# Kernel optimization log

Hardware: AMD Instinct MI355X
Metric: run time of the kernel (lower is better)

Reference implementation:

```python
import jax, jax.numpy as jnp
import numpy as np

DIM = 192
HEADS = 6
HEAD_DIM = DIM // HEADS
WS = 8            # window size
N = WS * WS       # tokens per window
IN_CC = 16        # top-k kept keys per query
B, H, W = 8, 64, 64
NEG = -100.0      # value used by the torch code for masked logits
EPS_NORM = 1e-12  # F.normalize eps
EPS_LN = 1e-5     # nn.LayerNorm eps


def _rel_pos_index(ws):
    coords = np.stack(np.meshgrid(np.arange(ws), np.arange(ws), indexing='ij'))  # (2,ws,ws)
    cf = coords.reshape(2, -1)
    rel = (cf[:, :, None] - cf[:, None, :]).transpose(1, 2, 0).astype(np.int64)  # (N,N,2)
    rel[:, :, 0] += ws - 1
    rel[:, :, 1] += ws - 1
    rel[:, :, 0] *= 2 * ws - 1
    return jnp.asarray(rel.sum(-1))  # (N,N) indices into (2ws-1)^2 table

REL_IDX = _rel_pos_index(WS)


def _layer_norm(x, g, b):
    mu = jnp.mean(x, -1, keepdims=True)
    var = jnp.mean(jnp.square(x - mu), -1, keepdims=True)
    return (x - mu) * jax.lax.rsqrt(var + EPS_LN) * g + b


def _l2n(x):
    n = jnp.sqrt(jnp.sum(jnp.square(x), -1, keepdims=True))
    return x / jnp.maximum(n, EPS_NORM)


def setup_inputs() -> dict:
    key = jax.random.key(0)
    ks = jax.random.split(key, 8)
    s = 0.02
    return {
        'x': jax.random.normal(ks[0], (B, DIM, H, W), jnp.float32),
        'norm1_g': jnp.ones((DIM,), jnp.float32),
        'norm1_b': jnp.zeros((DIM,), jnp.float32),
        'qkv_w': jax.random.normal(ks[1], (3 * DIM, DIM), jnp.float32) * s,
        'qkv_b': jnp.zeros((3 * DIM,), jnp.float32),
        'proj_w': jax.random.normal(ks[2], (DIM, DIM), jnp.float32) * s,
        'proj_b': jnp.zeros((DIM,), jnp.float32),
        'rpb_table': jax.random.normal(ks[3], ((2 * WS - 1) ** 2, HEADS), jnp.float32) * s,
        'temperature': jnp.ones((HEADS, 1, 1), jnp.float32),
        'norm2_g': jnp.ones((DIM,), jnp.float32),
        'norm2_b': jnp.zeros((DIM,), jnp.float32),
        'fc1_w': jax.random.normal(ks[4], (4 * DIM, DIM), jnp.float32) * s,
        'fc1_b': jnp.zeros((4 * DIM,), jnp.float32),
        'fc2_w': jax.random.normal(ks[5], (DIM, 4 * DIM), jnp.float32) * s,
        'fc2_b': jnp.zeros((DIM,), jnp.float32),
    }


def reference(x, norm1_g, norm1_b, qkv_w, qkv_b, proj_w, proj_b, rpb_table,
              temperature, norm2_g, norm2_b, fc1_w, fc1_b, fc2_w, fc2_b):
    b, c, h, w = x.shape
    # (B,C,H,W) -> (B,L,C), pre-norm (note: the torch code norms the shortcut too)
    xs = jnp.transpose(x.reshape(b, c, h * w), (0, 2, 1))
    shortcut = _layer_norm(xs, norm1_g, norm1_b)  # (B,L,C)

    # window partition: (B,H,W,C) -> (B*nWh*nWw, N, C); shift_size=0, no padding (H,W % WS == 0)
    xin = shortcut.reshape(b, h // WS, WS, w // WS, WS, c)
    xin = jnp.transpose(xin, (0, 1, 3, 2, 4, 5)).reshape(-1, N, c)
    B_ = xin.shape[0]

    qkv = (xin @ qkv_w.T + qkv_b).reshape(B_, N, 3, HEADS, HEAD_DIM)
    qkv = jnp.transpose(qkv, (2, 0, 3, 1, 4))  # (3, B_, h, N, d)
    q, k, v = qkv[0], qkv[1], qkv[2]

    # cosine attention with learned per-head temperature
    attn = jnp.einsum('bhnd,bhmd->bhnm', _l2n(q), _l2n(k)) * temperature  # (B_,h,N,N)

    # top-k sparsification: keep IN_CC largest logits per query (threshold == kth value;
    # equivalent to the torch topk+scatter mask for distinct values)
    kth = jax.lax.top_k(attn, IN_CC)[0][..., -1:]
    attn = jnp.where(attn >= kth, attn, NEG)

    # relative position bias gather: (N,N,h) -> (h,N,N)
    rpb = jnp.transpose(rpb_table[REL_IDX], (2, 0, 1))
    attn = jax.nn.softmax(attn + rpb[None], axis=-1)

    out = jnp.einsum('bhnm,bhmd->bhnd', attn, v)
    out = jnp.transpose(out, (0, 2, 1, 3)).reshape(B_, N, c)
    out = out @ proj_w.T + proj_b

    # window reverse -> (B, L, C)
    out = out.reshape(b, h // WS, w // WS, WS, WS, c)
    out = jnp.transpose(out, (0, 1, 3, 2, 4, 5)).reshape(b, h * w, c)

    x2 = shortcut + out  # drop_path = identity (eval)
    hdn = _layer_norm(x2, norm2_g, norm2_b)
    hdn = jax.nn.gelu(hdn @ fc1_w.T + fc1_b, approximate=False) @ fc2_w.T + fc2_b
    x2 = x2 + hdn

    # back to (B,C,H,W)
    return jnp.transpose(x2, (0, 2, 1)).reshape(b, c, h, w)
```

## Files before the change

### kernel.cpp

```cpp
#include <hip/hip_runtime.h>
#include <hip/hip_bf16.h>
#include <math.h>

#define DIM     192
#define HEADS   6
#define HEAD_DIM 32
#define NTOK    64
#define IN_CC   16
#define TTOT    32768
#define NWIN    512

using bf16x8 = __attribute__((ext_vector_type(8))) short;
using f32x4  = __attribute__((ext_vector_type(4))) float;
typedef unsigned short ushort_t;

__device__ __forceinline__ ushort_t f2b(float f) {
    unsigned u = __float_as_uint(f);
    u += 0x7fffu + ((u >> 16) & 1u);
    return (ushort_t)(u >> 16);
}
__device__ __forceinline__ unsigned pk2(float a, float b) {
    return (unsigned)f2b(a) | ((unsigned)f2b(b) << 16);
}
__device__ __forceinline__ float b2f(ushort_t u) {
    return __uint_as_float(((unsigned)u) << 16);
}

__global__ __launch_bounds__(256) void cvt_all_kernel(
    const float* __restrict__ s0, const float* __restrict__ s1,
    const float* __restrict__ s2, const float* __restrict__ s3,
    ushort_t* __restrict__ d0, ushort_t* __restrict__ d1,
    ushort_t* __restrict__ d2, ushort_t* __restrict__ d3)
{
    const int bid = blockIdx.x;
    const float* src; ushort_t* dst; int off, K;
    if (bid < 108)      { src = s0; dst = d0; off = bid;       K = 192; }
    else if (bid < 144) { src = s1; dst = d1; off = bid - 108; K = 192; }
    else if (bid < 288) { src = s2; dst = d2; off = bid - 144; K = 192; }
    else                { src = s3; dst = d3; off = bid - 288; K = 768; }
    const int K8 = K >> 3;
    const int d  = (off * 256 + threadIdx.x) * 4;
    const int frag = d >> 7, win = d & 127;
    const int m16w = win >> 3, k7 = win & 7;
    const int oblk = frag / K8, kblk = frag - oblk * K8;
    const int o = oblk * 16 + m16w, k = kblk * 8 + k7;
    float4 v = *(const float4*)(src + (size_t)o * K + k);
    ushort4 ov;
    ov.x = f2b(v.x); ov.y = f2b(v.y); ov.z = f2b(v.z); ov.w = f2b(v.w);
    *(ushort4*)(dst + d) = ov;
}

__global__ __launch_bounds__(256) void ln1_kernel(
    const float* __restrict__ x, const float* __restrict__ g,
    const float* __restrict__ bb, ushort_t* __restrict__ outh)
{
    __shared__ float xs[64][193];
    __shared__ float mu_s[64], rs_s[64];
    __shared__ float gs[192], bs[192];
    const int tid = threadIdx.x;
    const int t0  = blockIdx.x * 64;
    const int b   = t0 >> 12;
    const int hw0 = t0 & 4095;
    if (tid < 192) { gs[tid] = g[tid]; bs[tid] = bb[tid]; }
    const int tok = tid & 63, qq = tid >> 6;
    const float* xb = x + (size_t)b * (DIM * 4096) + hw0 + tok;
    #pragma unroll
    for (int it = 0; it < 48; ++it) {
        int c = it * 4 + qq;
        xs[tok][c] = xb[(size_t)c * 4096];
    }
    __syncthreads();
    const int tok2 = tid >> 2, p = tid & 3;
    float sum = 0.f;
    #pragma unroll
    for (int c = 0; c < 48; ++c) sum += xs[tok2][p * 48 + c];
    sum += __shfl_xor(sum, 1);
    sum += __shfl_xor(sum, 2);
    const float m = sum * (1.0f / 192.0f);
    float ss = 0.f;
    #pragma unroll
    for (int c = 0; c < 48; ++c) { float d = xs[tok2][p * 48 + c] - m; ss += d * d; }
    ss += __shfl_xor(ss, 1);
    ss += __shfl_xor(ss, 2);
    if (p == 0) {
        mu_s[tok2] = m;
        rs_s[tok2] = 1.0f / sqrtf(ss * (1.0f / 192.0f) + 1e-5f);
    }
    __syncthreads();
    ushort_t* obh = outh + (size_t)t0 * DIM;
    #pragma unroll
    for (int it = 0; it < 48; ++it) {
        int idx = it * 256 + tid;
        int tk = idx / 192, c = idx % 192;
        obh[idx] = f2b((xs[tk][c] - mu_s[tk]) * rs_s[tk] * gs[c] + bs[c]);
    }
}

__global__ __launch_bounds__(384) void attn_fused(
    const ushort_t* __restrict__ sc_h, const ushort_t* __restrict__ wqf,
    const float* __restrict__ qkv_b, const float* __restrict__ rpb_table,
    const float* __restrict__ temp, const ushort_t* __restrict__ wpf,
    const float* __restrict__ proj_b, float* __restrict__ x2)
{
    __shared__ __align__(16) char smem[98304];
    const int tid  = threadIdx.x;
    const int wave = tid >> 6, n = tid & 63;
    char* arena = smem + wave * 16384;
    ushort_t* Qh  = (ushort_t*)arena;
    ushort_t* Kh  = (ushort_t*)(arena + 5120);
    float*    Ss  = (float*)arena;
    ushort_t* Pl  = (ushort_t*)arena;
    ushort_t* Vt  = (ushort_t*)(arena + 10240);
    float*    ksb = (float*)(arena + 14848);
    float*    qnb = (float*)(arena + 15104);
    float*    rpb = (float*)(arena + 15360);
    ushort_t (*AoT)[200] = (ushort_t(*)[200])smem;
    float* Cww = (float*)(smem + 25600 + wave * 9216);

    const int win = blockIdx.x;
    const int h   = wave;
    const int b   = win >> 6;
    const int wh  = (win >> 3) & 7, ww = win & 7;
    const int i1  = n >> 3, j1 = n & 7;
    const int m16 = n & 15, quad = n >> 4;

    for (int r = n; r < 225; r += 64) rpb[r] = rpb_table[r * 6 + h];

    int trow[4];
    #pragma unroll
    for (int i = 0; i < 4; ++i) {
        const int row = 16 * i + m16;
        trow[i] = b * 4096 + (wh * 8 + (row >> 3)) * 64 + ww * 8 + (row & 7);
    }

    #pragma unroll
    for (int part = 0; part < 3; ++part) {
        const int o0 = part * 192 + h * 32;
        f32x4 pa[4][2];
        #pragma unroll
        for (int i = 0; i < 4; ++i)
            #pragma unroll
            for (int j = 0; j < 2; ++j)
                pa[i][j] = (f32x4)(0.0f);
        const ushort_t* Wb = wqf + (size_t)(o0 >> 4) * 24 * 128 + m16 * 8;
        for (int ks = 0; ks < 192; ks += 32) {
            bf16x8 af[4], wv[2];
            #pragma unroll
            for (int i = 0; i < 4; ++i)
                af[i] = *(const bf16x8*)(sc_h + (size_t)trow[i] * 192 + ks + quad * 8);
            #pragma unroll
            for (int j = 0; j < 2; ++j)
                wv[j] = *(const bf16x8*)(Wb + (size_t)(j * 24 + (ks >> 3) + quad) * 128);
            #pragma unroll
            for (int i = 0; i < 4; ++i)
                #pragma unroll
                for (int j = 0; j < 2; ++j)
                    pa[i][j] = __builtin_amdgcn_mfma_f32_16x16x32_bf16(wv[j], af[i], pa[i][j], 0, 0, 0);
        }
        float4 bv0 = *(const float4*)&qkv_b[o0 + quad * 4];
        float4 bv1 = *(const float4*)&qkv_b[o0 + 16 + quad * 4];
        float ssq[4] = {0.f, 0.f, 0.f, 0.f};
        #pragma unroll
        for (int i = 0; i < 4; ++i) {
            f32x4 v0 = pa[i][0], v1 = pa[i][1];
            v0[0] += bv0.x; v0[1] += bv0.y; v0[2] += bv0.z; v0[3] += bv0.w;
            v1[0] += bv1.x; v1[1] += bv1.y; v1[2] += bv1.z; v1[3] += bv1.w;
            if (part < 2) {
                #pragma unroll
                for (int r = 0; r < 4; ++r)
                    ssq[i] += v0[r] * v0[r] + v1[r] * v1[r];
                ushort_t* dst = (part == 0) ? Qh : Kh;
                uint2 w0, w1;
                w0.x = pk2(v0[0], v0[1]); w0.y = pk2(v0[2], v0[3]);
                w1.x = pk2(v1[0], v1[1]); w1.y = pk2(v1[2], v1[3]);
                *(uint2*)&dst[(16 * i + m16) * 40 + quad * 4]      = w0;
                *(uint2*)&dst[(16 * i + m16) * 40 + 16 + quad * 4] = w1;
            } else {
                #pragma unroll
                for (int r = 0; r < 4; ++r) {
                    Vt[(quad * 4 + r) * 72 + 4 * m16 + i]      = f2b(v0[r]);
                    Vt[(16 + quad * 4 + r) * 72 + 4 * m16 + i] = f2b(v1[r]);
                }
            }
        }
        if (part < 2) {
            #pragma unroll
            for (int i = 0; i < 4; ++i) {
                ssq[i] += __shfl_xor(ssq[i], 16);
                ssq[i] += __shfl_xor(ssq[i], 32);
            }
            if (quad == 0) {
                #pragma unroll
                for (int i = 0; i < 4; ++i) {
                    if (part == 0) qnb[16 * i + m16] = ssq[i];
                    else           ksb[4 * m16 + i]  = 1.0f / fmaxf(sqrtf(ssq[i]), 1e-12f);
                }
            }
        }
    }

    bf16x8 aq[4], bk[4];
    #pragma unroll
    for (int i = 0; i < 4; ++i) aq[i] = *(const bf16x8*)&Qh[(16*i + m16) * 40 + quad * 8];
    #pragma unroll
    for (int j = 0; j < 4; ++j) bk[j] = *(const bf16x8*)&Kh[(16*j + m16) * 40 + quad * 8];
    f32x4 acc[4][4];
    #pragma unroll
    for (int i = 0; i < 4; ++i)
        #pragma unroll
        for (int j = 0; j < 4; ++j)
            acc[i][j] = __builtin_amdgcn_mfma_f32_16x16x32_bf16(aq[i], bk[j], (f32x4)(0.0f), 0, 0, 0);

    float s[64];
    #pragma unroll
    for (int i = 0; i < 2; ++i)
        #pragma unroll
        for (int r = 0; r < 4; ++r) {
            f32x4 vv = { acc[i][0][r], acc[i][1][r], acc[i][2][r], acc[i][3][r] };
            *(f32x4*)&Ss[(16 * i + 4 * quad + r) * 68 + 4 * m16] = vv;
        }
    if (n < 32) {
        #pragma unroll
        for (int c = 0; c < 16; ++c)
            *(float4*)&s[4 * c] = *(const float4*)&Ss[n * 68 + 4 * c];
    }
    #pragma unroll
    for (int i = 2; i < 4; ++i)
        #pragma unroll
        for (int r = 0; r < 4; ++r) {
            f32x4 vv = { acc[i][0][r], acc[i][1][r], acc[i][2][r], acc[i][3][r] };
            *(f32x4*)&Ss[(16 * (i - 2) + 4 * quad + r) * 68 + 4 * m16] = vv;
        }
    if (n >= 32) {
        #pragma unroll
        for (int c = 0; c < 16; ++c)
            *(float4*)&s[4 * c] = *(const float4*)&Ss[(n - 32) * 68 + 4 * c];
    }

    const float qs = temp[h] / fmaxf(sqrtf(qnb[n]), 1e-12f);
    #pragma unroll
    for (int c = 0; c < 16; ++c) {
        float4 kv = *(const float4*)&ksb[4 * c];
        s[4*c+0] *= qs * kv.x; s[4*c+1] *= qs * kv.y;
        s[4*c+2] *= qs * kv.z; s[4*c+3] *= qs * kv.w;
    }

    float thr = 1e30f;
    for (int it = 0; it < IN_CC; ++it) {
        float mx = -1e30f;
        #pragma unroll
        for (int m = 0; m < 64; ++m) {
            float vv = (s[m] < thr) ? s[m] : -1e30f;
            mx = fmaxf(mx, vv);
        }
        thr = mx;
    }

    const int basen = i1 * 15 + j1;
    float mx = -1e30f;
    #pragma unroll
    for (int c = 0; c < 64; ++c) {
        const int m = 16 * (c & 3) + (c >> 2);
        const int i2 = m >> 3, j2 = m & 7;
        float vv = ((s[c] >= thr) ? s[c] : -100.0f)
                 + rpb[basen + (7 - i2) * 15 + (7 - j2)];
        s[c] = vv;
        mx = fmaxf(mx, vv);
    }
    float sum = 0.f;
    #pragma unroll
    for (int c = 0; c < 64; ++c) { float e = __expf(s[c] - mx); s[c] = e; sum += e; }
    const float inv = 1.0f / sum;
    #pragma unroll
    for (int c = 0; c < 64; ++c) s[c] *= inv;

    #pragma unroll
    for (int gix = 0; gix < 8; ++gix) {
        uint4 w;
        w.x = pk2(s[8*gix+0], s[8*gix+1]); w.y = pk2(s[8*gix+2], s[8*gix+3]);
        w.z = pk2(s[8*gix+4], s[8*gix+5]); w.w = pk2(s[8*gix+6], s[8*gix+7]);
        *(uint4*)&Pl[n * 72 + 8 * gix] = w;
    }

    f32x4 o[4][2];
    #pragma unroll
    for (int i = 0; i < 4; ++i)
        #pragma unroll
        for (int j2 = 0; j2 < 2; ++j2)
            o[i][j2] = (f32x4)(0.0f);
    #pragma unroll
    for (int kh = 0; kh < 64; kh += 32) {
        bf16x8 pa[4], vb[2];
        #pragma unroll
        for (int i = 0; i < 4; ++i)
            pa[i] = *(const bf16x8*)&Pl[(16*i + m16) * 72 + kh + quad * 8];
        #pragma unroll
        for (int j2 = 0; j2 < 2; ++j2)
            vb[j2] = *(const bf16x8*)&Vt[(16*j2 + m16) * 72 + kh + quad * 8];
        #pragma unroll
        for (int i = 0; i < 4; ++i)
            #pragma unroll
            for (int j2 = 0; j2 < 2; ++j2)
                o[i][j2] = __builtin_amdgcn_mfma_f32_16x16x32_bf16(pa[i], vb[j2], o[i][j2], 0, 0, 0);
    }
    __syncthreads();

    #pragma unroll
    for (int i = 0; i < 4; ++i) {
        #pragma unroll
        for (int r = 0; r < 4; ++r) {
            const int row = 16 * i + 4 * quad + r;
            AoT[row][h * 32 + m16]      = f2b(o[i][0][r]);
            AoT[row][h * 32 + 16 + m16] = f2b(o[i][1][r]);
        }
    }
    __syncthreads();

    f32x4 pacc[4][2];
    #pragma unroll
    for (int i = 0; i < 4; ++i)
        #pragma unroll
        for (int j = 0; j < 2; ++j)
            pacc[i][j] = (f32x4)(0.0f);
    const ushort_t* Wb = wpf + (size_t)(wave * 2) * 24 * 128 + m16 * 8;
    for (int ks = 0; ks < 192; ks += 32) {
        bf16x8 af[4], wv[2];
        #pragma unroll
        for (int i = 0; i < 4; ++i)
            af[i] = *(const bf16x8*)&AoT[16 * i + m16][quad * 8 + ks];
        #pragma unroll
        for (int j = 0; j < 2; ++j)
            wv[j] = *(const bf16x8*)(Wb + (size_t)(j * 24 + (ks >> 3) + quad) * 128);
        #pragma unroll
        for (int i = 0; i < 4; ++i)
            #pragma unroll
            for (int j = 0; j < 2; ++j)
                pacc[i][j] = __builtin_amdgcn_mfma_f32_16x16x32_bf16(wv[j], af[i], pacc[i][j], 0, 0, 0);
    }

    float4 bj[2];
    #pragma unroll
    for (int j = 0; j < 2; ++j)
        bj[j] = *(const float4*)&proj_b[wave * 32 + 16 * j + quad * 4];
    #pragma unroll
    for (int i = 0; i < 4; ++i)
        #pragma unroll
        for (int j = 0; j < 2; ++j) {
            f32x4 v = pacc[i][j];
            v[0] += bj[j].x; v[1] += bj[j].y; v[2] += bj[j].z; v[3] += bj[j].w;
            *(f32x4*)&Cww[(16 * i + m16) * 36 + 16 * j + quad * 4] = v;
        }

    #pragma unroll
    for (int q = 0; q < 8; ++q) {
        const int idx = q * 64 + n;
        const int row = idx >> 3, c4 = (idx & 7) * 4;
        const int ii = row >> 3, jj = row & 7;
        const int tt = b * 4096 + (wh * 8 + ii) * 64 + ww * 8 + jj;
        float4 vv = *(const float4*)&Cww[row * 36 + c4];
        uint2 rv = *(const uint2*)&sc_h[(size_t)tt * 192 + wave * 32 + c4];
        vv.x += b2f((ushort_t)(rv.x & 0xffffu));
        vv.y += b2f((ushort_t)(rv.x >> 16));
        vv.z += b2f((ushort_t)(rv.y & 0xffffu));
        vv.w += b2f((ushort_t)(rv.y >> 16));
        *(float4*)&x2[(size_t)tt * DIM + wave * 32 + c4] = vv;
    }
}

__global__ __launch_bounds__(256) void mlp_fused(
    const float* __restrict__ x2, const ushort_t* __restrict__ w1f,
    const ushort_t* __restrict__ w2f, const float* __restrict__ fc1_b,
    const float* __restrict__ fc2_b, const float* __restrict__ g2,
    const float* __restrict__ b2, float* __restrict__ outp)
{
    __shared__ __align__(16) char smem[43008];
    ushort_t (*h_h)[200] = (ushort_t(*)[200])smem;
    ushort_t (*a1c)[136] = (ushort_t(*)[136])(smem + 25600);
    float* gs  = (float*)(smem + 25600);
    float* bs  = gs + 192;

    const int tid  = threadIdx.x;
    const int wave = tid >> 6, lane = tid & 63;
    const int m16 = lane & 15, quad = lane >> 4;
    const int t0 = blockIdx.x * 64;
    const int b   = t0 >> 12;
    const int hw0 = t0 & 4095;

    if (tid < 192) { gs[tid] = g2[tid]; bs[tid] = b2[tid]; }
    __syncthreads();
    {
        const int tok = tid >> 2, p = tid & 3;
        const float* rp = x2 + (size_t)(t0 + tok) * DIM + p * 48;
        float xv[48];
        #pragma unroll
        for (int c4 = 0; c4 < 12; ++c4)
            *(float4*)&xv[c4 * 4] = *(const float4*)(rp + c4 * 4);
        float sum = 0.f;
        #pragma unroll
        for (int c = 0; c < 48; ++c) sum += xv[c];
        sum += __shfl_xor(sum, 1);
        sum += __shfl_xor(sum, 2);
        const float m = sum * (1.0f / 192.0f);
        float ss = 0.f;
        #pragma unroll
        for (int c = 0; c < 48; ++c) { float d = xv[c] - m; ss += d * d; }
        ss += __shfl_xor(ss, 1);
        ss += __shfl_xor(ss, 2);
        const float rs = 1.0f / sqrtf(ss * (1.0f / 192.0f) + 1e-5f);
        ushort_t* hp = &h_h[tok][p * 48];
        #pragma unroll
        for (int c2 = 0; c2 < 24; ++c2) {
            float v0 = (xv[2*c2]   - m) * rs * gs[p * 48 + 2*c2]   + bs[p * 48 + 2*c2];
            float v1 = (xv[2*c2+1] - m) * rs * gs[p * 48 + 2*c2+1] + bs[p * 48 + 2*c2+1];
            *(unsigned*)(hp + 2 * c2) = pk2(v0, v1);
        }
    }
    __syncthreads();

    f32x4 acc2[4][3];
    #pragma unroll
    for (int i = 0; i < 4; ++i)
        #pragma unroll
        for (int j = 0; j < 3; ++j)
            acc2[i][j] = (f32x4)(0.0f);

    for (int c = 0; c < 6; ++c) {
        f32x4 acc1[4][2];
        #pragma unroll
        for (int i = 0; i < 4; ++i)
            #pragma unroll
            for (int j = 0; j < 2; ++j)
                acc1[i][j] = (f32x4)(0.0f);
        const ushort_t* Wb1 = w1f + (size_t)(c * 8 + wave * 2) * 24 * 128 + m16 * 8;
        for (int ks = 0; ks < 192; ks += 32) {
            bf16x8 af[4], wv[2];
            #pragma unroll
            for (int i = 0; i < 4; ++i)
                af[i] = *(const bf16x8*)&h_h[16 * i + m16][quad * 8 + ks];
            #pragma unroll
            for (int j = 0; j < 2; ++j)
                wv[j] = *(const bf16x8*)(Wb1 + (size_t)(j * 24 + (ks >> 3) + quad) * 128);
            #pragma unroll
            for (int i = 0; i < 4; ++i)
                #pragma unroll
                for (int j = 0; j < 2; ++j)
                    acc1[i][j] = __builtin_amdgcn_mfma_f32_16x16x32_bf16(wv[j], af[i], acc1[i][j], 0, 0, 0);
        }
        #pragma unroll
        for (int j = 0; j < 2; ++j) {
            const int o = c * 128 + wave * 32 + 16 * j + quad * 4;
            const float4 bv = *(const float4*)&fc1_b[o];
            #pragma unroll
            for (int i = 0; i < 4; ++i) {
                f32x4 v = acc1[i][j];
                v[0] += bv.x; v[1] += bv.y; v[2] += bv.z; v[3] += bv.w;
                #pragma unroll
                for (int r = 0; r < 4; ++r) {
                    float xg = v[r];
                    float e1 = __expf(xg * (1.5957691f + 0.0713548f * xg * xg)) + 1.0f;
                    v[r] = xg - xg * __builtin_amdgcn_rcpf(e1);
                }
                uint2 pkd;
                pkd.x = pk2(v[0], v[1]); pkd.y = pk2(v[2], v[3]);
                *(uint2*)&a1c[16 * i + m16][wave * 32 + 16 * j + quad * 4] = pkd;
            }
        }
        __syncthreads();
        const ushort_t* Wb2 = w2f + (size_t)(wave * 3) * 96 * 128 + m16 * 8;
        for (int ks = 0; ks < 128; ks += 32) {
            bf16x8 af2[4], wv2[3];
            #pragma unroll
            for (int i = 0; i < 4; ++i)
                af2[i] = *(const bf16x8*)&a1c[16 * i + m16][quad * 8 + ks];
            #pragma unroll
            for (int j = 0; j < 3; ++j)
                wv2[j] = *(const bf16x8*)(Wb2 + (size_t)(j * 96 + c * 16 + (ks >> 3) + quad) * 128);
            #pragma unroll
            for (int i = 0; i < 4; ++i)
                #pragma unroll
                for (int j = 0; j < 3; ++j)
                    acc2[i][j] = __builtin_amdgcn_mfma_f32_16x16x32_bf16(wv2[j], af2[i], acc2[i][j], 0, 0, 0);
        }
        __syncthreads();
    }

    float (*Cw)[68] = (float(*)[68])(smem + wave * 8704);
    float4 b2j[3];
    #pragma unroll
    for (int j = 0; j < 3; ++j)
        b2j[j] = *(const float4*)&fc2_b[wave * 48 + 16 * j + quad * 4];
    #pragma unroll
    for (int p = 0; p < 2; ++p) {
        #pragma unroll
        for (int ih = 0; ih < 2; ++ih) {
            const int i = 2 * p + ih;
            #pragma unroll
            for (int j = 0; j < 3; ++j) {
                f32x4 v = acc2[i][j];
                v[0] += b2j[j].x; v[1] += b2j[j].y; v[2] += b2j[j].z; v[3] += b2j[j].w;
                *(f32x4*)&Cw[ih * 16 + m16][16 * j + quad * 4] = v;
            }
        }
        #pragma unroll
        for (int q = 0; q < 6; ++q) {
            const int idx = q * 64 + lane;
            const int cc = idx >> 3, t4 = (idx & 7) * 4;
            const int o  = wave * 48 + cc;
            const int tb = t0 + p * 32 + t4;
            float4 vv;
            vv.x = Cw[t4 + 0][cc] + x2[(size_t)(tb + 0) * DIM + o];
            vv.y = Cw[t4 + 1][cc] + x2[(size_t)(tb + 1) * DIM + o];
            vv.z = Cw[t4 + 2][cc] + x2[(size_t)(tb + 2) * DIM + o];
            vv.w = Cw[t4 + 3][cc] + x2[(size_t)(tb + 3) * DIM + o];
            *(float4*)&outp[(size_t)b * (DIM * 4096) + (size_t)o * 4096
                            + hw0 + p * 32 + t4] = vv;
        }
    }
}

extern "C" void kernel_launch(void* const* d_in, const int* in_sizes, int n_in,
                              void* d_out, int out_size, void* d_ws, size_t ws_size,
                              hipStream_t stream)
{
    const float* x        = (const float*)d_in[0];
    const float* norm1_g  = (const float*)d_in[1];
    const float* norm1_b  = (const float*)d_in[2];
    const float* qkv_w    = (const float*)d_in[3];
    const float* qkv_b    = (const float*)d_in[4];
    const float* proj_w   = (const float*)d_in[5];
    const float* proj_b   = (const float*)d_in[6];
    const float* rpbt     = (const float*)d_in[7];
    const float* temp     = (const float*)d_in[8];
    const float* norm2_g  = (const float*)d_in[9];
    const float* norm2_b  = (const float*)d_in[10];
    const float* fc1_w    = (const float*)d_in[11];
    const float* fc1_b    = (const float*)d_in[12];
    const float* fc2_w    = (const float*)d_in[13];
    const float* fc2_b    = (const float*)d_in[14];
    float* out = (float*)d_out;

    char* wsb = (char*)d_ws;
    ushort_t* shortcut_h = (ushort_t*)wsb;
    float*    x2         = (float*)(wsb + 12582912);
    ushort_t* wq  = (ushort_t*)(wsb + 125829120);
    ushort_t* wp  = wq + 110592;
    ushort_t* w1  = wp + 36864;
    ushort_t* w2  = w1 + 147456;

    hipLaunchKernelGGL(cvt_all_kernel, dim3(432), dim3(256), 0, stream,
                       qkv_w, proj_w, fc1_w, fc2_w, wq, wp, w1, w2);

    hipLaunchKernelGGL(ln1_kernel, dim3(TTOT / 64), dim3(256), 0, stream,
                       x, norm1_g, norm1_b, shortcut_h);
    hipLaunchKernelGGL(attn_fused, dim3(NWIN), dim3(384), 0, stream,
                       shortcut_h, wq, qkv_b, rpbt, temp, wp, proj_b, x2);
    hipLaunchKernelGGL(mlp_fused, dim3(TTOT / 64), dim3(256), 0, stream,
                       x2, w1, w2, fc1_b, fc2_b, norm2_g, norm2_b, out);
}
```

Measured before the change: 211.4 us.

## Keep Q/K fragments in registers via weight permutation and shrink attention LDS

The qkv weight rows for Q and K are permuted during bf16 conversion so that each lane's MFMA output forms a contiguous 8-element fragment. Q and K can then be packed straight into registers as MFMA operands, with no LDS round-trip. The score and probability staging buffers, along with the projection epilogue buffer, are cut to quarter- or half-size chunks processed in turns. This lowers shared memory from 96KB to about 62KB and sets launch_bounds to allow more resident blocks. The trade-offs are more serialized chunk steps, higher register pressure under the occupancy hint, and output-side work now depending on the permuted weight layout.

```diff
diff --git a/kernel.cpp b/kernel.cpp
--- a/kernel.cpp
+++ b/kernel.cpp
@@ -33,8 +33,8 @@
     ushort_t* __restrict__ d2, ushort_t* __restrict__ d3)
 {
     const int bid = blockIdx.x;
-    const float* src; ushort_t* dst; int off, K;
-    if (bid < 108)      { src = s0; dst = d0; off = bid;       K = 192; }
+    const float* src; ushort_t* dst; int off, K; bool perm = false;
+    if (bid < 108)      { src = s0; dst = d0; off = bid;       K = 192; perm = true; }
     else if (bid < 144) { src = s1; dst = d1; off = bid - 108; K = 192; }
     else if (bid < 288) { src = s2; dst = d2; off = bid - 144; K = 192; }
     else                { src = s3; dst = d3; off = bid - 288; K = 768; }
@@ -44,7 +44,13 @@
     const int m16w = win >> 3, k7 = win & 7;
     const int oblk = frag / K8, kblk = frag - oblk * K8;
     const int o = oblk * 16 + m16w, k = kblk * 8 + k7;
-    float4 v = *(const float4*)(src + (size_t)o * K + k);
+    int so = o;
+    if (perm && o < 384) {
+        const int s = o & 31;
+        const int c = (((s >> 2) & 3) << 3) | (((s >> 4) & 1) << 2) | (s & 3);
+        so = (o & ~31) | c;
+    }
+    float4 v = *(const float4*)(src + (size_t)so * K + k);
     ushort4 ov;
     ov.x = f2b(v.x); ov.y = f2b(v.y); ov.z = f2b(v.z); ov.w = f2b(v.w);
     *(ushort4*)(dst + d) = ov;
@@ -96,26 +102,24 @@
     }
 }
 
-__global__ __launch_bounds__(384) void attn_fused(
+__global__ __launch_bounds__(384, 3) void attn_fused(
     const ushort_t* __restrict__ sc_h, const ushort_t* __restrict__ wqf,
     const float* __restrict__ qkv_b, const float* __restrict__ rpb_table,
     const float* __restrict__ temp, const ushort_t* __restrict__ wpf,
     const float* __restrict__ proj_b, float* __restrict__ x2)
 {
-    __shared__ __align__(16) char smem[98304];
+    __shared__ __align__(16) char smem[63840];
     const int tid  = threadIdx.x;
     const int wave = tid >> 6, n = tid & 63;
-    char* arena = smem + wave * 16384;
-    ushort_t* Qh  = (ushort_t*)arena;
-    ushort_t* Kh  = (ushort_t*)(arena + 5120);
-    float*    Ss  = (float*)arena;
-    ushort_t* Pl  = (ushort_t*)arena;
-    ushort_t* Vt  = (ushort_t*)(arena + 10240);
-    float*    ksb = (float*)(arena + 14848);
-    float*    qnb = (float*)(arena + 15104);
-    float*    rpb = (float*)(arena + 15360);
+    char* arena = smem + wave * 9728;
+    float*    Ssq = (float*)arena;
+    ushort_t* Ph  = (ushort_t*)arena;
+    ushort_t* Vt  = (ushort_t*)(arena + 4608);
+    float*    ksb = (float*)(arena + 9216);
+    float*    qnb = (float*)(arena + 9472);
+    float*    rpb = (float*)(smem + 58368) + wave * 228;
     ushort_t (*AoT)[200] = (ushort_t(*)[200])smem;
-    float* Cww = (float*)(smem + 25600 + wave * 9216);
+    float* Cwj = (float*)(smem + 25600 + wave * 5120);
 
     const int win = blockIdx.x;
     const int h   = wave;
@@ -133,6 +137,7 @@
         trow[i] = b * 4096 + (wh * 8 + (row >> 3)) * 64 + ww * 8 + (row & 7);
     }
 
+    bf16x8 qA[4], kB[4];
     #pragma unroll
     for (int part = 0; part < 3; ++part) {
         const int o0 = part * 192 + h * 32;
@@ -157,25 +162,46 @@
                 for (int j = 0; j < 2; ++j)
                     pa[i][j] = __builtin_amdgcn_mfma_f32_16x16x32_bf16(wv[j], af[i], pa[i][j], 0, 0, 0);
         }
-        float4 bv0 = *(const float4*)&qkv_b[o0 + quad * 4];
-        float4 bv1 = *(const float4*)&qkv_b[o0 + 16 + quad * 4];
-        float ssq[4] = {0.f, 0.f, 0.f, 0.f};
-        #pragma unroll
-        for (int i = 0; i < 4; ++i) {
-            f32x4 v0 = pa[i][0], v1 = pa[i][1];
-            v0[0] += bv0.x; v0[1] += bv0.y; v0[2] += bv0.z; v0[3] += bv0.w;
-            v1[0] += bv1.x; v1[1] += bv1.y; v1[2] += bv1.z; v1[3] += bv1.w;
-            if (part < 2) {
-                #pragma unroll
-                for (int r = 0; r < 4; ++r)
-                    ssq[i] += v0[r] * v0[r] + v1[r] * v1[r];
-                ushort_t* dst = (part == 0) ? Qh : Kh;
-                uint2 w0, w1;
-                w0.x = pk2(v0[0], v0[1]); w0.y = pk2(v0[2], v0[3]);
-                w1.x = pk2(v1[0], v1[1]); w1.y = pk2(v1[2], v1[3]);
-                *(uint2*)&dst[(16 * i + m16) * 40 + quad * 4]      = w0;
-                *(uint2*)&dst[(16 * i + m16) * 40 + 16 + quad * 4] = w1;
-            } else {
+        if (part < 2) {
+            const float4 bv0 = *(const float4*)&qkv_b[o0 + 8 * quad];
+            const float4 bv1 = *(const float4*)&qkv_b[o0 + 8 * quad + 4];
+            float ssq[4];
+            #pragma unroll
+            for (int i = 0; i < 4; ++i) {
+                f32x4 v0 = pa[i][0], v1 = pa[i][1];
+                v0[0] += bv0.x; v0[1] += bv0.y; v0[2] += bv0.z; v0[3] += bv0.w;
+                v1[0] += bv1.x; v1[1] += bv1.y; v1[2] += bv1.z; v1[3] += bv1.w;
+                float sq = 0.f;
+                #pragma unroll
+                for (int r = 0; r < 4; ++r) sq += v0[r] * v0[r] + v1[r] * v1[r];
+                ssq[i] = sq;
+                bf16x8 fr;
+                fr[0] = (short)f2b(v0[0]); fr[1] = (short)f2b(v0[1]);
+                fr[2] = (short)f2b(v0[2]); fr[3] = (short)f2b(v0[3]);
+                fr[4] = (short)f2b(v1[0]); fr[5] = (short)f2b(v1[1]);
+                fr[6] = (short)f2b(v1[2]); fr[7] = (short)f2b(v1[3]);
+                if (part == 0) qA[i] = fr; else kB[i] = fr;
+            }
+            #pragma unroll
+            for (int i = 0; i < 4; ++i) {
+                ssq[i] += __shfl_xor(ssq[i], 16);
+                ssq[i] += __shfl_xor(ssq[i], 32);
+            }
+            if (quad == 0) {
+                #pragma unroll
+                for (int i = 0; i < 4; ++i) {
+                    if (part == 0) qnb[16 * i + m16] = ssq[i];
+                    else           ksb[4 * m16 + i]  = 1.0f / fmaxf(sqrtf(ssq[i]), 1e-12f);
+                }
+            }
+        } else {
+            const float4 bv0 = *(const float4*)&qkv_b[o0 + quad * 4];
+            const float4 bv1 = *(const float4*)&qkv_b[o0 + 16 + quad * 4];
+            #pragma unroll
+            for (int i = 0; i < 4; ++i) {
+                f32x4 v0 = pa[i][0], v1 = pa[i][1];
+                v0[0] += bv0.x; v0[1] += bv0.y; v0[2] += bv0.z; v0[3] += bv0.w;
+                v1[0] += bv1.x; v1[1] += bv1.y; v1[2] += bv1.z; v1[3] += bv1.w;
                 #pragma unroll
                 for (int r = 0; r < 4; ++r) {
                     Vt[(quad * 4 + r) * 72 + 4 * m16 + i]      = f2b(v0[r]);
@@ -183,58 +209,28 @@
                 }
             }
         }
-        if (part < 2) {
-            #pragma unroll
-            for (int i = 0; i < 4; ++i) {
-                ssq[i] += __shfl_xor(ssq[i], 16);
-                ssq[i] += __shfl_xor(ssq[i], 32);
-            }
-            if (quad == 0) {
-                #pragma unroll
-                for (int i = 0; i < 4; ++i) {
-                    if (part == 0) qnb[16 * i + m16] = ssq[i];
-                    else           ksb[4 * m16 + i]  = 1.0f / fmaxf(sqrtf(ssq[i]), 1e-12f);
-                }
-            }
-        }
-    }
-
-    bf16x8 aq[4], bk[4];
-    #pragma unroll
-    for (int i = 0; i < 4; ++i) aq[i] = *(const bf16x8*)&Qh[(16*i + m16) * 40 + quad * 8];
-    #pragma unroll
-    for (int j = 0; j < 4; ++j) bk[j] = *(const bf16x8*)&Kh[(16*j + m16) * 40 + quad * 8];
+    }
+
     f32x4 acc[4][4];
     #pragma unroll
     for (int i = 0; i < 4; ++i)
         #pragma unroll
         for (int j = 0; j < 4; ++j)
-            acc[i][j] = __builtin_amdgcn_mfma_f32_16x16x32_bf16(aq[i], bk[j], (f32x4)(0.0f), 0, 0, 0);
+            acc[i][j] = __builtin_amdgcn_mfma_f32_16x16x32_bf16(qA[i], kB[j], (f32x4)(0.0f), 0, 0, 0);
 
     float s[64];
     #pragma unroll
-    for (int i = 0; i < 2; ++i)
+    for (int i = 0; i < 4; ++i) {
         #pragma unroll
         for (int r = 0; r < 4; ++r) {
             f32x4 vv = { acc[i][0][r], acc[i][1][r], acc[i][2][r], acc[i][3][r] };
-            *(f32x4*)&Ss[(16 * i + 4 * quad + r) * 68 + 4 * m16] = vv;
-        }
-    if (n < 32) {
-        #pragma unroll
-        for (int c = 0; c < 16; ++c)
-            *(float4*)&s[4 * c] = *(const float4*)&Ss[n * 68 + 4 * c];
-    }
-    #pragma unroll
-    for (int i = 2; i < 4; ++i)
-        #pragma unroll
-        for (int r = 0; r < 4; ++r) {
-            f32x4 vv = { acc[i][0][r], acc[i][1][r], acc[i][2][r], acc[i][3][r] };
-            *(f32x4*)&Ss[(16 * (i - 2) + 4 * quad + r) * 68 + 4 * m16] = vv;
-        }
-    if (n >= 32) {
-        #pragma unroll
-        for (int c = 0; c < 16; ++c)
-            *(float4*)&s[4 * c] = *(const float4*)&Ss[(n - 32) * 68 + 4 * c];
+            *(f32x4*)&Ssq[(4 * quad + r) * 68 + 4 * m16] = vv;
+        }
+        if ((n >> 4) == i) {
+            #pragma unroll
+            for (int c = 0; c < 16; ++c)
+                *(float4*)&s[4 * c] = *(const float4*)&Ssq[(n & 15) * 68 + 4 * c];
+        }
     }
 
     const float qs = temp[h] / fmaxf(sqrtf(qnb[n]), 1e-12f);
@@ -274,13 +270,12 @@
     #pragma unroll
     for (int c = 0; c < 64; ++c) s[c] *= inv;
 
-    #pragma unroll
-    for (int gix = 0; gix < 8; ++gix) {
-        uint4 w;
-        w.x = pk2(s[8*gix+0], s[8*gix+1]); w.y = pk2(s[8*gix+2], s[8*gix+3]);
-        w.z = pk2(s[8*gix+4], s[8*gix+5]); w.w = pk2(s[8*gix+6], s[8*gix+7]);
-        *(uint4*)&Pl[n * 72 + 8 * gix] = w;
-    }
+    bf16x8 vb[2][2];
+    #pragma unroll
+    for (int kh2 = 0; kh2 < 2; ++kh2)
+        #pragma unroll
+        for (int j2 = 0; j2 < 2; ++j2)
+            vb[kh2][j2] = *(const bf16x8*)&Vt[(16 * j2 + m16) * 72 + kh2 * 32 + quad * 8];
 
     f32x4 o[4][2];
     #pragma unroll
@@ -289,19 +284,26 @@
         for (int j2 = 0; j2 < 2; ++j2)
             o[i][j2] = (f32x4)(0.0f);
     #pragma unroll
-    for (int kh = 0; kh < 64; kh += 32) {
-        bf16x8 pa[4], vb[2];
-        #pragma unroll
-        for (int i = 0; i < 4; ++i)
-            pa[i] = *(const bf16x8*)&Pl[(16*i + m16) * 72 + kh + quad * 8];
-        #pragma unroll
-        for (int j2 = 0; j2 < 2; ++j2)
-            vb[j2] = *(const bf16x8*)&Vt[(16*j2 + m16) * 72 + kh + quad * 8];
-        #pragma unroll
-        for (int i = 0; i < 4; ++i)
-            #pragma unroll
-            for (int j2 = 0; j2 < 2; ++j2)
-                o[i][j2] = __builtin_amdgcn_mfma_f32_16x16x32_bf16(pa[i], vb[j2], o[i][j2], 0, 0, 0);
+    for (int hf = 0; hf < 2; ++hf) {
+        if ((n >> 5) == hf) {
+            #pragma unroll
+            for (int g = 0; g < 8; ++g) {
+                uint4 w;
+                w.x = pk2(s[8*g+0], s[8*g+1]); w.y = pk2(s[8*g+2], s[8*g+3]);
+                w.z = pk2(s[8*g+4], s[8*g+5]); w.w = pk2(s[8*g+6], s[8*g+7]);
+                *(uint4*)&Ph[(n & 31) * 72 + 8 * g] = w;
+            }
+        }
+        #pragma unroll
+        for (int ih = 0; ih < 2; ++ih) {
+            const int i = 2 * hf + ih;
+            #pragma unroll
+            for (int kh2 = 0; kh2 < 2; ++kh2) {
+                bf16x8 pafr = *(const bf16x8*)&Ph[(16 * ih + m16) * 72 + kh2 * 32 + quad * 8];
+                o[i][0] = __builtin_amdgcn_mfma_f32_16x16x32_bf16(pafr, vb[kh2][0], o[i][0], 0, 0, 0);
+                o[i][1] = __builtin_amdgcn_mfma_f32_16x16x32_bf16(pafr, vb[kh2][1], o[i][1], 0, 0, 0);
+            }
+        }
     }
     __syncthreads();
 
@@ -338,32 +340,30 @@
                 pacc[i][j] = __builtin_amdgcn_mfma_f32_16x16x32_bf16(wv[j], af[i], pacc[i][j], 0, 0, 0);
     }
 
-    float4 bj[2];
-    #pragma unroll
-    for (int j = 0; j < 2; ++j)
-        bj[j] = *(const float4*)&proj_b[wave * 32 + 16 * j + quad * 4];
-    #pragma unroll
-    for (int i = 0; i < 4; ++i)
-        #pragma unroll
-        for (int j = 0; j < 2; ++j) {
+    #pragma unroll
+    for (int j = 0; j < 2; ++j) {
+        const float4 bj = *(const float4*)&proj_b[wave * 32 + 16 * j + quad * 4];
+        #pragma unroll
+        for (int i = 0; i < 4; ++i) {
             f32x4 v = pacc[i][j];
-            v[0] += bj[j].x; v[1] += bj[j].y; v[2] += bj[j].z; v[3] += bj[j].w;
-            *(f32x4*)&Cww[(16 * i + m16) * 36 + 16 * j + quad * 4] = v;
-        }
-
-    #pragma unroll
-    for (int q = 0; q < 8; ++q) {
-        const int idx = q * 64 + n;
-        const int row = idx >> 3, c4 = (idx & 7) * 4;
-        const int ii = row >> 3, jj = row & 7;
-        const int tt = b * 4096 + (wh * 8 + ii) * 64 + ww * 8 + jj;
-        float4 vv = *(const float4*)&Cww[row * 36 + c4];
-        uint2 rv = *(const uint2*)&sc_h[(size_t)tt * 192 + wave * 32 + c4];
-        vv.x += b2f((ushort_t)(rv.x & 0xffffu));
-        vv.y += b2f((ushort_t)(rv.x >> 16));
-        vv.z += b2f((ushort_t)(rv.y & 0xffffu));
-        vv.w += b2f((ushort_t)(rv.y >> 16));
-        *(float4*)&x2[(size_t)tt * DIM + wave * 32 + c4] = vv;
+            v[0] += bj.x; v[1] += bj.y; v[2] += bj.z; v[3] += bj.w;
+            *(f32x4*)&Cwj[(16 * i + m16) * 20 + quad * 4] = v;
+        }
+        #pragma unroll
+        for (int q = 0; q < 4; ++q) {
+            const int idx = q * 64 + n;
+            const int row = idx >> 2, c4 = (idx & 3) * 4;
+            const int ii = row >> 3, jj = row & 7;
+            const int tt = b * 4096 + (wh * 8 + ii) * 64 + ww * 8 + jj;
+            const int oc = wave * 32 + 16 * j + c4;
+            float4 vv = *(const float4*)&Cwj[row * 20 + c4];
+            uint2 rv = *(const uint2*)&sc_h[(size_t)tt * 192 + oc];
+            vv.x += b2f((ushort_t)(rv.x & 0xffffu));
+            vv.y += b2f((ushort_t)(rv.x >> 16));
+            vv.z += b2f((ushort_t)(rv.y & 0xffffu));
+            vv.w += b2f((ushort_t)(rv.y >> 16));
+            *(float4*)&x2[(size_t)tt * DIM + oc] = vv;
+        }
     }
 }
 
```

Result: slower. 225.6 us (+6.7%).
